# Kernel tuning notes

Hardware: AMD Instinct MI355X
Metric: run time of the kernel (lower is better)

## Reference

```python
import jax, jax.numpy as jnp
import numpy as np

N = 20000
IN_C = 512
HID = 64
H1 = 8
OUT_C = 256
E = 320000
NEG_SLOPE = 0.2


def gat_conv(x, src, dst, W, a_src, a_dst, b, concat):
    # PyG GATConv (shared lin for src/dst), inference mode (no dropout).
    H, C = a_src.shape
    h = (x @ W).reshape(N, H, C)                      # [N,H,C]
    alpha_src = (h * a_src[None]).sum(-1)             # [N,H]
    alpha_dst = (h * a_dst[None]).sum(-1)             # [N,H]
    alpha = jax.nn.leaky_relu(alpha_src[src] + alpha_dst[dst], NEG_SLOPE)  # [E,H]
    # segment softmax over incoming edges of each dst node
    amax = jax.ops.segment_max(alpha, dst, num_segments=N)
    amax = jnp.where(jnp.isfinite(amax), amax, 0.0)
    ex = jnp.exp(alpha - amax[dst])
    denom = jax.ops.segment_sum(ex, dst, num_segments=N)
    coef = ex / (denom[dst] + 1e-16)                  # [E,H]
    msg = h[src] * coef[:, :, None]                   # [E,H,C]
    out = jax.ops.segment_sum(msg, dst, num_segments=N)  # [N,H,C]
    out = out.reshape(N, H * C) if concat else out.mean(axis=1)
    return out + b


def setup_inputs() -> dict:
    key = jax.random.key(0)
    ks = jax.random.split(key, 10)
    x = jax.random.normal(ks[0], (N, IN_C), dtype=jnp.float32)
    edge_index = jax.random.randint(ks[1], (2, E), 0, N, dtype=jnp.int32)
    s1 = 1.0 / np.sqrt(IN_C)
    s2 = 1.0 / np.sqrt(HID * H1)
    W1 = jax.random.uniform(ks[2], (IN_C, H1 * HID), jnp.float32, -s1, s1)
    att_src1 = jax.random.uniform(ks[3], (H1, HID), jnp.float32, -s1, s1)
    att_dst1 = jax.random.uniform(ks[4], (H1, HID), jnp.float32, -s1, s1)
    b1 = jnp.zeros((H1 * HID,), jnp.float32)
    W2 = jax.random.uniform(ks[5], (H1 * HID, OUT_C), jnp.float32, -s2, s2)
    att_src2 = jax.random.uniform(ks[6], (1, OUT_C), jnp.float32, -s2, s2)
    att_dst2 = jax.random.uniform(ks[7], (1, OUT_C), jnp.float32, -s2, s2)
    b2 = jnp.zeros((OUT_C,), jnp.float32)
    return {"x": x, "edge_index": edge_index, "W1": W1, "att_src1": att_src1,
            "att_dst1": att_dst1, "b1": b1, "W2": W2, "att_src2": att_src2,
            "att_dst2": att_dst2, "b2": b2}


def reference(x, edge_index, W1, att_src1, att_dst1, b1, W2, att_src2, att_dst2, b2):
    # add self-loops (PyG GATConv default add_self_loops=True)
    loop = jnp.arange(N, dtype=edge_index.dtype)
    src = jnp.concatenate([edge_index[0], loop])
    dst = jnp.concatenate([edge_index[1], loop])
    h = gat_conv(x, src, dst, W1, att_src1, att_dst1, b1, concat=True)
    h = jax.nn.elu(h)
    out = gat_conv(h, src, dst, W2, att_src2, att_dst2, b2, concat=False)
    return jax.nn.log_softmax(out, axis=1)
```

## Files before the change

### kernel.cpp

```cpp
#include <hip/hip_runtime.h>
#include <math.h>

#define N_NODES 20000
#define IN_CH   512
#define HID_TOT 512
#define OUT_CH  256
#define N_EDGE  320000
#define TOT_EDGE (N_EDGE + N_NODES)
#define EPAD    400000

typedef __attribute__((ext_vector_type(8))) short short8;
typedef __attribute__((ext_vector_type(4))) float f32x4;
typedef __attribute__((ext_vector_type(2))) float f32x2;

__device__ __forceinline__ ushort f2bf(float f) {
    union { float f; unsigned u; } v; v.f = f;
    unsigned u = v.u;
    return (ushort)((u + 0x7fffu + ((u >> 16) & 1u)) >> 16);
}

__device__ __forceinline__ void glds16(const ushort* g, ushort* l) {
    __builtin_amdgcn_global_load_lds(
        (const __attribute__((address_space(1))) void*)g,
        (__attribute__((address_space(3))) void*)l, 16, 0, 0);
}

__device__ __forceinline__ float lrelu(float a) { return fmaxf(a, 0.2f * a); }

#define NA_BLK (N_NODES * IN_CH / 4 / 256)
#define NB_BLK ((IN_CH / 64) * (HID_TOT / 4))
#define NC_BLK ((HID_TOT / 64) * (OUT_CH / 4))
#define NZ_BLK ((N_NODES + 255) / 256)
__global__ __launch_bounds__(256) void prep_kernel(const float* __restrict__ x,
                                                   ushort* __restrict__ xb,
                                                   const float* __restrict__ W1,
                                                   ushort* __restrict__ w1t,
                                                   const float* __restrict__ W2,
                                                   ushort* __restrict__ w2t,
                                                   int* __restrict__ counts,
                                                   float* __restrict__ as2,
                                                   float* __restrict__ ad2) {
    int b = blockIdx.x;
    int t = threadIdx.x;
    if (b < NA_BLK) {
        int i = b * 256 + t;
        float4 v = *(const float4*)&x[(size_t)i * 4];
        ushort4 o = make_ushort4(f2bf(v.x), f2bf(v.y), f2bf(v.z), f2bf(v.w));
        *(ushort4*)&xb[(size_t)i * 4] = o;
    } else if (b < NA_BLK + NB_BLK) {
        int bb = b - NA_BLK;
        int k = (bb & 7) * 64 + (t & 63);
        int n = (bb >> 3) * 4 + (t >> 6);
        w1t[(size_t)n * IN_CH + k] = f2bf(W1[(size_t)k * HID_TOT + n]);
    } else if (b < NA_BLK + NB_BLK + NC_BLK) {
        int bb = b - NA_BLK - NB_BLK;
        int k = (bb & 7) * 64 + (t & 63);
        int n = (bb >> 3) * 4 + (t >> 6);
        w2t[(size_t)n * HID_TOT + k] = f2bf(W2[(size_t)k * OUT_CH + n]);
    } else {
        int i = (b - NA_BLK - NB_BLK - NC_BLK) * 256 + t;
        if (i < N_NODES) { counts[i] = 0; as2[i] = 0.f; ad2[i] = 0.f; }
    }
}

__global__ void hist_kernel(const int* __restrict__ ei, int* __restrict__ counts) {
    int e = blockIdx.x * blockDim.x + threadIdx.x;
    if (e >= TOT_EDGE) return;
    int d = (e < N_EDGE) ? ei[N_EDGE + e] : (e - N_EDGE);
    atomicAdd(&counts[d], 1);
}

__global__ __launch_bounds__(1024) void scan_kernel(const int* __restrict__ counts,
                                                    int* __restrict__ offsets,
                                                    int* __restrict__ cursors) {
    const int C = (N_NODES + 1023) / 1024;
    int t = threadIdx.x;
    int lane = t & 63, wid = t >> 6;
    int base = t * C;
    int sum = 0;
#pragma unroll
    for (int i = 0; i < C; i++) {
        int idx = base + i;
        if (idx < N_NODES) sum += (counts[idx] + 3) & ~3;
    }
    int val = sum;
#pragma unroll
    for (int off = 1; off < 64; off <<= 1) {
        int y = __shfl_up(val, off);
        if (lane >= off) val += y;
    }
    __shared__ int wsum[16], woff[16], stotal;
    if (lane == 63) wsum[wid] = val;
    __syncthreads();
    if (t == 0) {
        int r = 0;
        for (int w = 0; w < 16; w++) { woff[w] = r; r += wsum[w]; }
        stotal = r;
    }
    __syncthreads();
    int running = woff[wid] + (val - sum);
#pragma unroll
    for (int i = 0; i < C; i++) {
        int idx = base + i;
        if (idx < N_NODES) {
            offsets[idx] = running;
            cursors[idx] = running;
            running += (counts[idx] + 3) & ~3;
        }
    }
    if (t == 0) offsets[N_NODES] = stotal;
}

__global__ void scatter_kernel(const int* __restrict__ ei, int* __restrict__ cursors,
                               int* __restrict__ srcs, int* __restrict__ dsts) {
    int e = blockIdx.x * blockDim.x + threadIdx.x;
    if (e >= TOT_EDGE) return;
    int s, d;
    if (e < N_EDGE) { s = ei[e]; d = ei[N_EDGE + e]; } else { s = e - N_EDGE; d = s; }
    int pos = atomicAdd(&cursors[d], 1);
    srcs[pos] = s;
    dsts[pos] = d;
}

__global__ void pad_kernel(const int* __restrict__ cursors, const int* __restrict__ offsets,
                           int* __restrict__ srcs, int* __restrict__ dsts) {
    int v = blockIdx.x * blockDim.x + threadIdx.x;
    if (v >= N_NODES) return;
    int a = cursors[v], b = offsets[v + 1];
    for (int p = a; p < b; p++) { srcs[p] = 0; dsts[p] = -1; }
}

__global__ __launch_bounds__(256, 2) void gemm_mfma_kernel(const ushort* __restrict__ A,
                                                           const ushort* __restrict__ Bt,
                                                           unsigned char* __restrict__ Cf8,
                                                           const float* __restrict__ asrc,
                                                           const float* __restrict__ adst,
                                                           float* __restrict__ as_out,
                                                           float* __restrict__ ad_out,
                                                           int M, int N, int K, int layer1) {
    __shared__ ushort As[128 * 64];
    __shared__ ushort Bs[128 * 64];
    int t = threadIdx.x;
    int lane = t & 63;
    int wave = t >> 6;
    int wr = (wave >> 1) * 64;
    int wc = (wave & 1) * 64;
    int bm = blockIdx.y * 128, bn = blockIdx.x * 128;
    int q = lane >> 4, l15 = lane & 15;

    const ushort* Aptr[4]; ushort* Alds[4];
    const ushort* Bptr[4]; ushort* Blds[4];
#pragma unroll
    for (int k = 0; k < 4; k++) {
        int c = t + 256 * k;
        int r = c >> 3, kqs = c & 7;
        int kqg = kqs ^ (r & 7);
        int ar = bm + r; if (ar >= M) ar = M - 1;
        Aptr[k] = A + (size_t)ar * K + kqg * 8;
        Alds[k] = &As[c * 8];
        Bptr[k] = Bt + (size_t)(bn + r) * K + kqg * 8;
        Blds[k] = &Bs[c * 8];
    }

    f32x4 acc[4][4];
#pragma unroll
    for (int i = 0; i < 4; i++)
#pragma unroll
        for (int j = 0; j < 4; j++) acc[i][j] = f32x4{0.f, 0.f, 0.f, 0.f};

    for (int k0 = 0; k0 < K; k0 += 64) {
        __syncthreads();
        glds16(Aptr[0] + k0, Alds[0]);
        glds16(Aptr[1] + k0, Alds[1]);
        glds16(Aptr[2] + k0, Alds[2]);
        glds16(Aptr[3] + k0, Alds[3]);
        glds16(Bptr[0] + k0, Blds[0]);
        glds16(Bptr[1] + k0, Blds[1]);
        glds16(Bptr[2] + k0, Blds[2]);
        glds16(Bptr[3] + k0, Blds[3]);
        __syncthreads();

#pragma unroll
        for (int s = 0; s < 2; s++) {
            int kq = s * 4 + q;
            short8 af[4], bf[4];
#pragma unroll
            for (int i = 0; i < 4; i++) {
                int row = wr + i * 16 + l15;
                int slot = kq ^ (row & 7);
                af[i] = *(const short8*)&As[row * 64 + slot * 8];
            }
#pragma unroll
            for (int j = 0; j < 4; j++) {
                int row = wc + j * 16 + l15;
                int slot = kq ^ (row & 7);
                bf[j] = *(const short8*)&Bs[row * 64 + slot * 8];
            }
#pragma unroll
            for (int i = 0; i < 4; i++)
#pragma unroll
                for (int j = 0; j < 4; j++)
                    acc[i][j] = __builtin_amdgcn_mfma_f32_16x16x32_bf16(af[i], bf[j], acc[i][j], 0, 0, 0);
        }
    }

    float av[4], dv[4];
#pragma unroll
    for (int j = 0; j < 4; j++) {
        int cg = bn + wc + j * 16 + l15;
        av[j] = asrc[cg];
        dv[j] = adst[cg];
    }
    float ps[4][4], pd[4][4];
#pragma unroll
    for (int i = 0; i < 4; i++)
#pragma unroll
        for (int r = 0; r < 4; r++) {
            float p = 0.f, d = 0.f;
#pragma unroll
            for (int j = 0; j < 4; j++) {
                p = fmaf(acc[i][j][r], av[j], p);
                d = fmaf(acc[i][j][r], dv[j], d);
            }
            ps[i][r] = p; pd[i][r] = d;
        }
#pragma unroll
    for (int off = 1; off < 16; off <<= 1) {
#pragma unroll
        for (int i = 0; i < 4; i++)
#pragma unroll
            for (int r = 0; r < 4; r++) {
                ps[i][r] += __shfl_xor(ps[i][r], off);
                pd[i][r] += __shfl_xor(pd[i][r], off);
            }
    }

    int hidx = blockIdx.x * 2 + (wave & 1);
#pragma unroll
    for (int i = 0; i < 4; i++) {
#pragma unroll
        for (int r = 0; r < 4; r++) {
            int rg = bm + wr + i * 16 + q * 4 + r;
            if (rg < M) {
#pragma unroll
                for (int j = 0; j < 4; j++) {
                    int cg = bn + wc + j * 16 + l15;
                    int w8 = __builtin_amdgcn_cvt_pk_fp8_f32(acc[i][j][r], acc[i][j][r], 0, false);
                    Cf8[(size_t)rg * N + cg] = (unsigned char)(w8 & 0xff);
                }
                if (l15 == 0) {
                    if (layer1) {
                        as_out[rg * 8 + hidx] = ps[i][r];
                        ad_out[rg * 8 + hidx] = pd[i][r];
                    } else {
                        atomicAdd(&as_out[rg], ps[i][r]);
                        atomicAdd(&ad_out[rg], pd[i][r]);
                    }
                }
            }
        }
    }
}

__global__ __launch_bounds__(256) void wk1_kernel(const int* __restrict__ srcs,
                                                  const int* __restrict__ dsts,
                                                  const float* __restrict__ as1,
                                                  const float* __restrict__ ad1,
                                                  const int* __restrict__ offsets,
                                                  float* __restrict__ w1) {
    int pos = blockIdx.x * 256 + threadIdx.x;
    int tot = offsets[N_NODES];
    if (pos >= tot) return;
    int d = dsts[pos];
    if (d < 0) {
#pragma unroll
        for (int h = 0; h < 8; h++) w1[h * EPAD + pos] = 0.f;
        return;
    }
    int s = srcs[pos];
    float4 a0 = *(const float4*)&as1[(size_t)s * 8];
    float4 a1 = *(const float4*)&as1[(size_t)s * 8 + 4];
    float4 d0 = *(const float4*)&ad1[(size_t)d * 8];
    float4 d1 = *(const float4*)&ad1[(size_t)d * 8 + 4];
    w1[0 * EPAD + pos] = __expf(lrelu(a0.x + d0.x));
    w1[1 * EPAD + pos] = __expf(lrelu(a0.y + d0.y));
    w1[2 * EPAD + pos] = __expf(lrelu(a0.z + d0.z));
    w1[3 * EPAD + pos] = __expf(lrelu(a0.w + d0.w));
    w1[4 * EPAD + pos] = __expf(lrelu(a1.x + d1.x));
    w1[5 * EPAD + pos] = __expf(lrelu(a1.y + d1.y));
    w1[6 * EPAD + pos] = __expf(lrelu(a1.z + d1.z));
    w1[7 * EPAD + pos] = __expf(lrelu(a1.w + d1.w));
}

__global__ __launch_bounds__(256) void wk2_kernel(const int* __restrict__ srcs,
                                                  const int* __restrict__ dsts,
                                                  const float* __restrict__ as2,
                                                  const float* __restrict__ ad2,
                                                  const int* __restrict__ offsets,
                                                  float* __restrict__ w2) {
    int pos = blockIdx.x * 256 + threadIdx.x;
    int tot = offsets[N_NODES];
    if (pos >= tot) return;
    int d = dsts[pos];
    if (d < 0) { w2[pos] = 0.f; return; }
    w2[pos] = __expf(lrelu(as2[srcs[pos]] + ad2[d]));
}

__global__ __launch_bounds__(64) void agg1_kernel(const unsigned char* __restrict__ h1f,
                                                  const float* __restrict__ w1,
                                                  const int* __restrict__ offsets,
                                                  const int* __restrict__ srcs,
                                                  const float* __restrict__ b1,
                                                  ushort* __restrict__ h1ab) {
    int b = blockIdx.x;
    int head = b & 7;
    int grp = b >> 3;
    int lane = threadIdx.x;
    int sub = lane >> 3;
    int l8 = lane & 7;
    int v = grp * 8 + sub;
    int cofs = head * 64 + l8 * 8;
    const unsigned char* hb = h1f + cofs;
    const float* wh = w1 + head * EPAD;
    int s = offsets[v], e = offsets[v + 1];

    float denom = 0.f;
    float acc[8];
#pragma unroll
    for (int k = 0; k < 8; k++) acc[k] = 0.f;

    int i = s;
    for (; i + 8 <= e; i += 8) {
        int4 s0 = *(const int4*)&srcs[i];
        int4 s1 = *(const int4*)&srcs[i + 4];
        float4 w0 = *(const float4*)&wh[i];
        float4 w1v = *(const float4*)&wh[i + 4];
        uint2 r[8];
        r[0] = *(const uint2*)&hb[(size_t)s0.x * HID_TOT];
        r[1] = *(const uint2*)&hb[(size_t)s0.y * HID_TOT];
        r[2] = *(const uint2*)&hb[(size_t)s0.z * HID_TOT];
        r[3] = *(const uint2*)&hb[(size_t)s0.w * HID_TOT];
        r[4] = *(const uint2*)&hb[(size_t)s1.x * HID_TOT];
        r[5] = *(const uint2*)&hb[(size_t)s1.y * HID_TOT];
        r[6] = *(const uint2*)&hb[(size_t)s1.z * HID_TOT];
        r[7] = *(const uint2*)&hb[(size_t)s1.w * HID_TOT];
        float ww[8] = {w0.x, w0.y, w0.z, w0.w, w1v.x, w1v.y, w1v.z, w1v.w};
        denom += (w0.x + w0.y) + (w0.z + w0.w) + (w1v.x + w1v.y) + (w1v.z + w1v.w);
#pragma unroll
        for (int j = 0; j < 8; j++) {
            f32x2 pa = __builtin_amdgcn_cvt_pk_f32_fp8(r[j].x, false);
            f32x2 pb = __builtin_amdgcn_cvt_pk_f32_fp8(r[j].x, true);
            f32x2 pc = __builtin_amdgcn_cvt_pk_f32_fp8(r[j].y, false);
            f32x2 pdd = __builtin_amdgcn_cvt_pk_f32_fp8(r[j].y, true);
            acc[0] = fmaf(ww[j], pa.x, acc[0]); acc[1] = fmaf(ww[j], pa.y, acc[1]);
            acc[2] = fmaf(ww[j], pb.x, acc[2]); acc[3] = fmaf(ww[j], pb.y, acc[3]);
            acc[4] = fmaf(ww[j], pc.x, acc[4]); acc[5] = fmaf(ww[j], pc.y, acc[5]);
            acc[6] = fmaf(ww[j], pdd.x, acc[6]); acc[7] = fmaf(ww[j], pdd.y, acc[7]);
        }
    }
    if (i < e) {
        int4 s0 = *(const int4*)&srcs[i];
        float4 w0 = *(const float4*)&wh[i];
        uint2 r[4];
        r[0] = *(const uint2*)&hb[(size_t)s0.x * HID_TOT];
        r[1] = *(const uint2*)&hb[(size_t)s0.y * HID_TOT];
        r[2] = *(const uint2*)&hb[(size_t)s0.z * HID_TOT];
        r[3] = *(const uint2*)&hb[(size_t)s0.w * HID_TOT];
        float ww[4] = {w0.x, w0.y, w0.z, w0.w};
        denom += (w0.x + w0.y) + (w0.z + w0.w);
#pragma unroll
        for (int j = 0; j < 4; j++) {
            f32x2 pa = __builtin_amdgcn_cvt_pk_f32_fp8(r[j].x, false);
            f32x2 pb = __builtin_amdgcn_cvt_pk_f32_fp8(r[j].x, true);
            f32x2 pc = __builtin_amdgcn_cvt_pk_f32_fp8(r[j].y, false);
            f32x2 pdd = __builtin_amdgcn_cvt_pk_f32_fp8(r[j].y, true);
            acc[0] = fmaf(ww[j], pa.x, acc[0]); acc[1] = fmaf(ww[j], pa.y, acc[1]);
            acc[2] = fmaf(ww[j], pb.x, acc[2]); acc[3] = fmaf(ww[j], pb.y, acc[3]);
            acc[4] = fmaf(ww[j], pc.x, acc[4]); acc[5] = fmaf(ww[j], pc.y, acc[5]);
            acc[6] = fmaf(ww[j], pdd.x, acc[6]); acc[7] = fmaf(ww[j], pdd.y, acc[7]);
        }
    }

    float inv = 1.f / (denom + 1e-16f);
    short8 ov;
#pragma unroll
    for (int k = 0; k < 8; k++) {
        float o = acc[k] * inv + b1[cofs + k];
        o = (o > 0.f) ? o : expm1f(o);
        ov[k] = (short)f2bf(o);
    }
    *(short8*)&h1ab[(size_t)v * HID_TOT + cofs] = ov;
}

__global__ __launch_bounds__(64) void agg2_kernel(const unsigned char* __restrict__ h2f,
                                                  const float* __restrict__ w2,
                                                  const int* __restrict__ offsets,
                                                  const int* __restrict__ srcs,
                                                  const float* __restrict__ b2,
                                                  float* __restrict__ out) {
    int lane = threadIdx.x;
    int sub = lane >> 5;
    int l32 = lane & 31;
    int v = blockIdx.x * 2 + sub;
    int c8 = l32 * 8;
    const unsigned char* hb = h2f + c8;
    int s = offsets[v], e = offsets[v + 1];

    float denom = 0.f;
    float acc[8];
#pragma unroll
    for (int k = 0; k < 8; k++) acc[k] = 0.f;

    int i = s;
    for (; i + 8 <= e; i += 8) {
        int4 s0 = *(const int4*)&srcs[i];
        int4 s1 = *(const int4*)&srcs[i + 4];
        float4 w0 = *(const float4*)&w2[i];
        float4 w1v = *(const float4*)&w2[i + 4];
        uint2 r[8];
        r[0] = *(const uint2*)&hb[(size_t)s0.x * OUT_CH];
        r[1] = *(const uint2*)&hb[(size_t)s0.y * OUT_CH];
        r[2] = *(const uint2*)&hb[(size_t)s0.z * OUT_CH];
        r[3] = *(const uint2*)&hb[(size_t)s0.w * OUT_CH];
        r[4] = *(const uint2*)&hb[(size_t)s1.x * OUT_CH];
        r[5] = *(const uint2*)&hb[(size_t)s1.y * OUT_CH];
        r[6] = *(const uint2*)&hb[(size_t)s1.z * OUT_CH];
        r[7] = *(const uint2*)&hb[(size_t)s1.w * OUT_CH];
        float ww[8] = {w0.x, w0.y, w0.z, w0.w, w1v.x, w1v.y, w1v.z, w1v.w};
        denom += (w0.x + w0.y) + (w0.z + w0.w) + (w1v.x + w1v.y) + (w1v.z + w1v.w);
#pragma unroll
        for (int j = 0; j < 8; j++) {
            f32x2 pa = __builtin_amdgcn_cvt_pk_f32_fp8(r[j].x, false);
            f32x2 pb = __builtin_amdgcn_cvt_pk_f32_fp8(r[j].x, true);
            f32x2 pc = __builtin_amdgcn_cvt_pk_f32_fp8(r[j].y, false);
            f32x2 pdd = __builtin_amdgcn_cvt_pk_f32_fp8(r[j].y, true);
            acc[0] = fmaf(ww[j], pa.x, acc[0]); acc[1] = fmaf(ww[j], pa.y, acc[1]);
            acc[2] = fmaf(ww[j], pb.x, acc[2]); acc[3] = fmaf(ww[j], pb.y, acc[3]);
            acc[4] = fmaf(ww[j], pc.x, acc[4]); acc[5] = fmaf(ww[j], pc.y, acc[5]);
            acc[6] = fmaf(ww[j], pdd.x, acc[6]); acc[7] = fmaf(ww[j], pdd.y, acc[7]);
        }
    }
    if (i < e) {
        int4 s0 = *(const int4*)&srcs[i];
        float4 w0 = *(const float4*)&w2[i];
        uint2 r[4];
        r[0] = *(const uint2*)&hb[(size_t)s0.x * OUT_CH];
        r[1] = *(const uint2*)&hb[(size_t)s0.y * OUT_CH];
        r[2] = *(const uint2*)&hb[(size_t)s0.z * OUT_CH];
        r[3] = *(const uint2*)&hb[(size_t)s0.w * OUT_CH];
        float ww[4] = {w0.x, w0.y, w0.z, w0.w};
        denom += (w0.x + w0.y) + (w0.z + w0.w);
#pragma unroll
        for (int j = 0; j < 4; j++) {
            f32x2 pa = __builtin_amdgcn_cvt_pk_f32_fp8(r[j].x, false);
            f32x2 pb = __builtin_amdgcn_cvt_pk_f32_fp8(r[j].x, true);
            f32x2 pc = __builtin_amdgcn_cvt_pk_f32_fp8(r[j].y, false);
            f32x2 pdd = __builtin_amdgcn_cvt_pk_f32_fp8(r[j].y, true);
            acc[0] = fmaf(ww[j], pa.x, acc[0]); acc[1] = fmaf(ww[j], pa.y, acc[1]);
            acc[2] = fmaf(ww[j], pb.x, acc[2]); acc[3] = fmaf(ww[j], pb.y, acc[3]);
            acc[4] = fmaf(ww[j], pc.x, acc[4]); acc[5] = fmaf(ww[j], pc.y, acc[5]);
            acc[6] = fmaf(ww[j], pdd.x, acc[6]); acc[7] = fmaf(ww[j], pdd.y, acc[7]);
        }
    }

    float inv = 1.f / (denom + 1e-16f);
    float xv[8];
#pragma unroll
    for (int k = 0; k < 8; k++) xv[k] = acc[k] * inv + b2[c8 + k];

    float mm = xv[0];
#pragma unroll
    for (int k = 1; k < 8; k++) mm = fmaxf(mm, xv[k]);
#pragma unroll
    for (int off = 1; off < 32; off <<= 1) mm = fmaxf(mm, __shfl_xor(mm, off));
    float sum = 0.f;
#pragma unroll
    for (int k = 0; k < 8; k++) sum += __expf(xv[k] - mm);
#pragma unroll
    for (int off = 1; off < 32; off <<= 1) sum += __shfl_xor(sum, off);
    float ls = logf(sum);
    float4 o0, o1;
    o0.x = xv[0] - mm - ls; o0.y = xv[1] - mm - ls;
    o0.z = xv[2] - mm - ls; o0.w = xv[3] - mm - ls;
    o1.x = xv[4] - mm - ls; o1.y = xv[5] - mm - ls;
    o1.z = xv[6] - mm - ls; o1.w = xv[7] - mm - ls;
    *(float4*)&out[(size_t)v * OUT_CH + c8] = o0;
    *(float4*)&out[(size_t)v * OUT_CH + c8 + 4] = o1;
}

static inline size_t align256(size_t x) { return (x + 255) & ~(size_t)255; }

extern "C" void kernel_launch(void* const* d_in, const int* in_sizes, int n_in,
                              void* d_out, int out_size, void* d_ws, size_t ws_size,
                              hipStream_t stream) {
    const float* x    = (const float*)d_in[0];
    const int*   ei   = (const int*)d_in[1];
    const float* W1   = (const float*)d_in[2];
    const float* as1w = (const float*)d_in[3];
    const float* ad1w = (const float*)d_in[4];
    const float* b1   = (const float*)d_in[5];
    const float* W2   = (const float*)d_in[6];
    const float* as2w = (const float*)d_in[7];
    const float* ad2w = (const float*)d_in[8];
    const float* b2   = (const float*)d_in[9];
    float* out = (float*)d_out;

    char* p = (char*)d_ws;
    unsigned char* h1f = (unsigned char*)p; p += align256((size_t)N_NODES * HID_TOT);
    unsigned char* h2f = (unsigned char*)p; p += align256((size_t)N_NODES * OUT_CH);
    ushort* xb   = (ushort*)p; p += align256(sizeof(ushort) * (size_t)N_NODES * IN_CH);
    ushort* h1ab = xb;
    ushort* w1t  = (ushort*)p; p += align256(sizeof(ushort) * (size_t)IN_CH * HID_TOT);
    ushort* w2t  = (ushort*)p; p += align256(sizeof(ushort) * (size_t)HID_TOT * OUT_CH);
    float* as1  = (float*)p; p += align256(sizeof(float) * (size_t)N_NODES * 8);
    float* ad1  = (float*)p; p += align256(sizeof(float) * (size_t)N_NODES * 8);
    float* as2  = (float*)p; p += align256(sizeof(float) * (size_t)N_NODES);
    float* ad2  = (float*)p; p += align256(sizeof(float) * (size_t)N_NODES);
    int* counts  = (int*)p; p += align256(sizeof(int) * (size_t)N_NODES);
    int* offsets = (int*)p; p += align256(sizeof(int) * (size_t)(N_NODES + 1));
    int* cursors = (int*)p; p += align256(sizeof(int) * (size_t)N_NODES);
    int* srcs    = (int*)p; p += align256(sizeof(int) * (size_t)EPAD);
    int* dsts    = (int*)p; p += align256(sizeof(int) * (size_t)EPAD);
    float* w1    = (float*)p; p += align256(sizeof(float) * (size_t)EPAD * 8);
    float* w2    = (float*)p; p += align256(sizeof(float) * (size_t)EPAD);

    prep_kernel<<<NA_BLK + NB_BLK + NC_BLK + NZ_BLK, 256, 0, stream>>>(
        x, xb, W1, w1t, W2, w2t, counts, as2, ad2);

    int eb = (TOT_EDGE + 255) / 256;
    hist_kernel<<<eb, 256, 0, stream>>>(ei, counts);
    scan_kernel<<<1, 1024, 0, stream>>>(counts, offsets, cursors);
    scatter_kernel<<<eb, 256, 0, stream>>>(ei, cursors, srcs, dsts);
    pad_kernel<<<(N_NODES + 255) / 256, 256, 0, stream>>>(cursors, offsets, srcs, dsts);

    int wb = (EPAD + 255) / 256;
    gemm_mfma_kernel<<<dim3(HID_TOT / 128, (N_NODES + 127) / 128), 256, 0, stream>>>(
        xb, w1t, h1f, as1w, ad1w, as1, ad1, N_NODES, HID_TOT, IN_CH, 1);
    wk1_kernel<<<wb, 256, 0, stream>>>(srcs, dsts, as1, ad1, offsets, w1);
    agg1_kernel<<<2500 * 8, 64, 0, stream>>>(h1f, w1, offsets, srcs, b1, h1ab);

    gemm_mfma_kernel<<<dim3(OUT_CH / 128, (N_NODES + 127) / 128), 256, 0, stream>>>(
        h1ab, w2t, h2f, as2w, ad2w, as2, ad2, N_NODES, OUT_CH, HID_TOT, 0);
    wk2_kernel<<<wb, 256, 0, stream>>>(srcs, dsts, as2, ad2, offsets, w2);
    agg2_kernel<<<N_NODES / 2, 64, 0, stream>>>(h2f, w2, offsets, srcs, b2, out);
}
```

Before: 284.9 us.

## Fuse edge-weight computation into aggregation kernels and degree-sort node order

Removes the separate wk1/wk2 kernels that wrote per-edge exp weights to global memory; each aggregation lane now computes one edge's weight from head-major attention scores and broadcasts it by shuffle. Padding slots point to a sentinel node with a -1e30 score and zero features, which removes the dsts array and the pad kernel. The scan kernel also builds a degree-bucketed permutation so each block processes nodes of similar degree, reducing divergence. It also adds software prefetch of the next source indices. This cuts global traffic and launches at the cost of extra exp and shuffle work inside the aggregation loops.

```diff
diff --git a/kernel.cpp b/kernel.cpp
--- a/kernel.cpp
+++ b/kernel.cpp
@@ -2,6 +2,7 @@
 #include <math.h>
 
 #define N_NODES 20000
+#define NP1     20001
 #define IN_CH   512
 #define HID_TOT 512
 #define OUT_CH  256
@@ -38,8 +39,11 @@
                                                    const float* __restrict__ W2,
                                                    ushort* __restrict__ w2t,
                                                    int* __restrict__ counts,
+                                                   float* __restrict__ as1,
                                                    float* __restrict__ as2,
-                                                   float* __restrict__ ad2) {
+                                                   float* __restrict__ ad2,
+                                                   unsigned char* __restrict__ h1f,
+                                                   unsigned char* __restrict__ h2f) {
     int b = blockIdx.x;
     int t = threadIdx.x;
     if (b < NA_BLK) {
@@ -60,6 +64,10 @@
     } else {
         int i = (b - NA_BLK - NB_BLK - NC_BLK) * 256 + t;
         if (i < N_NODES) { counts[i] = 0; as2[i] = 0.f; ad2[i] = 0.f; }
+        if (i == N_NODES) as2[N_NODES] = -1e30f;
+        if (i < 8) as1[(size_t)i * NP1 + N_NODES] = -1e30f;
+        if (i < 128) ((unsigned*)(h1f + (size_t)N_NODES * HID_TOT))[i] = 0u;
+        if (i < 64)  ((unsigned*)(h2f + (size_t)N_NODES * OUT_CH))[i] = 0u;
     }
 }
 
@@ -72,7 +80,9 @@
 
 __global__ __launch_bounds__(1024) void scan_kernel(const int* __restrict__ counts,
                                                     int* __restrict__ offsets,
-                                                    int* __restrict__ cursors) {
+                                                    int* __restrict__ cursors,
+                                                    int* __restrict__ srcs,
+                                                    int* __restrict__ perm) {
     const int C = (N_NODES + 1023) / 1024;
     int t = threadIdx.x;
     int lane = t & 63, wid = t >> 6;
@@ -90,7 +100,9 @@
         if (lane >= off) val += y;
     }
     __shared__ int wsum[16], woff[16], stotal;
+    __shared__ int bins[64];
     if (lane == 63) wsum[wid] = val;
+    if (t < 64) bins[t] = 0;
     __syncthreads();
     if (t == 0) {
         int r = 0;
@@ -105,29 +117,48 @@
         if (idx < N_NODES) {
             offsets[idx] = running;
             cursors[idx] = running;
-            running += (counts[idx] + 3) & ~3;
+            int real = counts[idx];
+            int padded = (real + 3) & ~3;
+            for (int pp = running + real; pp < running + padded; pp++)
+                srcs[pp] = N_NODES;
+            running += padded;
         }
     }
     if (t == 0) offsets[N_NODES] = stotal;
+
+#pragma unroll
+    for (int i = 0; i < C; i++) {
+        int idx = base + i;
+        if (idx < N_NODES) {
+            int d = counts[idx]; if (d > 63) d = 63;
+            atomicAdd(&bins[d], 1);
+        }
+    }
+    __syncthreads();
+    if (t == 0) {
+        int r = 0;
+        for (int d = 0; d < 64; d++) { int c = bins[d]; bins[d] = r; r += c; }
+    }
+    __syncthreads();
+#pragma unroll
+    for (int i = 0; i < C; i++) {
+        int idx = base + i;
+        if (idx < N_NODES) {
+            int d = counts[idx]; if (d > 63) d = 63;
+            int pos = atomicAdd(&bins[d], 1);
+            perm[pos] = idx;
+        }
+    }
 }
 
 __global__ void scatter_kernel(const int* __restrict__ ei, int* __restrict__ cursors,
-                               int* __restrict__ srcs, int* __restrict__ dsts) {
+                               int* __restrict__ srcs) {
     int e = blockIdx.x * blockDim.x + threadIdx.x;
     if (e >= TOT_EDGE) return;
     int s, d;
     if (e < N_EDGE) { s = ei[e]; d = ei[N_EDGE + e]; } else { s = e - N_EDGE; d = s; }
     int pos = atomicAdd(&cursors[d], 1);
     srcs[pos] = s;
-    dsts[pos] = d;
-}
-
-__global__ void pad_kernel(const int* __restrict__ cursors, const int* __restrict__ offsets,
-                           int* __restrict__ srcs, int* __restrict__ dsts) {
-    int v = blockIdx.x * blockDim.x + threadIdx.x;
-    if (v >= N_NODES) return;
-    int a = cursors[v], b = offsets[v + 1];
-    for (int p = a; p < b; p++) { srcs[p] = 0; dsts[p] = -1; }
 }
 
 __global__ __launch_bounds__(256, 2) void gemm_mfma_kernel(const ushort* __restrict__ A,
@@ -250,8 +281,8 @@
                 }
                 if (l15 == 0) {
                     if (layer1) {
-                        as_out[rg * 8 + hidx] = ps[i][r];
-                        ad_out[rg * 8 + hidx] = pd[i][r];
+                        as_out[(size_t)hidx * NP1 + rg] = ps[i][r];
+                        ad_out[(size_t)hidx * NP1 + rg] = pd[i][r];
                     } else {
                         atomicAdd(&as_out[rg], ps[i][r]);
                         atomicAdd(&ad_out[rg], pd[i][r]);
@@ -262,54 +293,12 @@
     }
 }
 
-__global__ __launch_bounds__(256) void wk1_kernel(const int* __restrict__ srcs,
-                                                  const int* __restrict__ dsts,
+__global__ __launch_bounds__(64) void agg1_kernel(const unsigned char* __restrict__ h1f,
                                                   const float* __restrict__ as1,
                                                   const float* __restrict__ ad1,
                                                   const int* __restrict__ offsets,
-                                                  float* __restrict__ w1) {
-    int pos = blockIdx.x * 256 + threadIdx.x;
-    int tot = offsets[N_NODES];
-    if (pos >= tot) return;
-    int d = dsts[pos];
-    if (d < 0) {
-#pragma unroll
-        for (int h = 0; h < 8; h++) w1[h * EPAD + pos] = 0.f;
-        return;
-    }
-    int s = srcs[pos];
-    float4 a0 = *(const float4*)&as1[(size_t)s * 8];
-    float4 a1 = *(const float4*)&as1[(size_t)s * 8 + 4];
-    float4 d0 = *(const float4*)&ad1[(size_t)d * 8];
-    float4 d1 = *(const float4*)&ad1[(size_t)d * 8 + 4];
-    w1[0 * EPAD + pos] = __expf(lrelu(a0.x + d0.x));
-    w1[1 * EPAD + pos] = __expf(lrelu(a0.y + d0.y));
-    w1[2 * EPAD + pos] = __expf(lrelu(a0.z + d0.z));
-    w1[3 * EPAD + pos] = __expf(lrelu(a0.w + d0.w));
-    w1[4 * EPAD + pos] = __expf(lrelu(a1.x + d1.x));
-    w1[5 * EPAD + pos] = __expf(lrelu(a1.y + d1.y));
-    w1[6 * EPAD + pos] = __expf(lrelu(a1.z + d1.z));
-    w1[7 * EPAD + pos] = __expf(lrelu(a1.w + d1.w));
-}
-
-__global__ __launch_bounds__(256) void wk2_kernel(const int* __restrict__ srcs,
-                                                  const int* __restrict__ dsts,
-                                                  const float* __restrict__ as2,
-                                                  const float* __restrict__ ad2,
-                                                  const int* __restrict__ offsets,
-                                                  float* __restrict__ w2) {
-    int pos = blockIdx.x * 256 + threadIdx.x;
-    int tot = offsets[N_NODES];
-    if (pos >= tot) return;
-    int d = dsts[pos];
-    if (d < 0) { w2[pos] = 0.f; return; }
-    w2[pos] = __expf(lrelu(as2[srcs[pos]] + ad2[d]));
-}
-
-__global__ __launch_bounds__(64) void agg1_kernel(const unsigned char* __restrict__ h1f,
-                                                  const float* __restrict__ w1,
-                                                  const int* __restrict__ offsets,
                                                   const int* __restrict__ srcs,
+                                                  const int* __restrict__ perm,
                                                   const float* __restrict__ b1,
                                                   ushort* __restrict__ h1ab) {
     int b = blockIdx.x;
@@ -318,10 +307,11 @@
     int lane = threadIdx.x;
     int sub = lane >> 3;
     int l8 = lane & 7;
-    int v = grp * 8 + sub;
+    int v = perm[grp * 8 + sub];
     int cofs = head * 64 + l8 * 8;
     const unsigned char* hb = h1f + cofs;
-    const float* wh = w1 + head * EPAD;
+    const float* as1h = as1 + (size_t)head * NP1;
+    float adv = ad1[(size_t)head * NP1 + v];
     int s = offsets[v], e = offsets[v + 1];
 
     float denom = 0.f;
@@ -330,22 +320,36 @@
     for (int k = 0; k < 8; k++) acc[k] = 0.f;
 
     int i = s;
-    for (; i + 8 <= e; i += 8) {
-        int4 s0 = *(const int4*)&srcs[i];
-        int4 s1 = *(const int4*)&srcs[i + 4];
-        float4 w0 = *(const float4*)&wh[i];
-        float4 w1v = *(const float4*)&wh[i + 4];
+    int4 cs0 = {0, 0, 0, 0}, cs1 = {0, 0, 0, 0};
+    int csn = N_NODES;
+    if (i + 8 <= e) {
+        cs0 = *(const int4*)&srcs[i];
+        cs1 = *(const int4*)&srcs[i + 4];
+        csn = srcs[i + l8];
+    }
+    while (i + 8 <= e) {
         uint2 r[8];
-        r[0] = *(const uint2*)&hb[(size_t)s0.x * HID_TOT];
-        r[1] = *(const uint2*)&hb[(size_t)s0.y * HID_TOT];
-        r[2] = *(const uint2*)&hb[(size_t)s0.z * HID_TOT];
-        r[3] = *(const uint2*)&hb[(size_t)s0.w * HID_TOT];
-        r[4] = *(const uint2*)&hb[(size_t)s1.x * HID_TOT];
-        r[5] = *(const uint2*)&hb[(size_t)s1.y * HID_TOT];
-        r[6] = *(const uint2*)&hb[(size_t)s1.z * HID_TOT];
-        r[7] = *(const uint2*)&hb[(size_t)s1.w * HID_TOT];
-        float ww[8] = {w0.x, w0.y, w0.z, w0.w, w1v.x, w1v.y, w1v.z, w1v.w};
-        denom += (w0.x + w0.y) + (w0.z + w0.w) + (w1v.x + w1v.y) + (w1v.z + w1v.w);
+        r[0] = *(const uint2*)&hb[(size_t)cs0.x * HID_TOT];
+        r[1] = *(const uint2*)&hb[(size_t)cs0.y * HID_TOT];
+        r[2] = *(const uint2*)&hb[(size_t)cs0.z * HID_TOT];
+        r[3] = *(const uint2*)&hb[(size_t)cs0.w * HID_TOT];
+        r[4] = *(const uint2*)&hb[(size_t)cs1.x * HID_TOT];
+        r[5] = *(const uint2*)&hb[(size_t)cs1.y * HID_TOT];
+        r[6] = *(const uint2*)&hb[(size_t)cs1.z * HID_TOT];
+        r[7] = *(const uint2*)&hb[(size_t)cs1.w * HID_TOT];
+        float aown = as1h[csn];
+        int ni = i + 8;
+        int4 ns0 = cs0, ns1 = cs1; int nsn = csn;
+        if (ni + 8 <= e) {
+            ns0 = *(const int4*)&srcs[ni];
+            ns1 = *(const int4*)&srcs[ni + 4];
+            nsn = srcs[ni + l8];
+        }
+        float w_own = __expf(lrelu(aown + adv));
+        denom += w_own;
+        float ww[8];
+#pragma unroll
+        for (int j = 0; j < 8; j++) ww[j] = __shfl(w_own, (lane & 56) | j);
 #pragma unroll
         for (int j = 0; j < 8; j++) {
             f32x2 pa = __builtin_amdgcn_cvt_pk_f32_fp8(r[j].x, false);
@@ -357,17 +361,21 @@
             acc[4] = fmaf(ww[j], pc.x, acc[4]); acc[5] = fmaf(ww[j], pc.y, acc[5]);
             acc[6] = fmaf(ww[j], pdd.x, acc[6]); acc[7] = fmaf(ww[j], pdd.y, acc[7]);
         }
+        cs0 = ns0; cs1 = ns1; csn = nsn; i = ni;
     }
     if (i < e) {
         int4 s0 = *(const int4*)&srcs[i];
-        float4 w0 = *(const float4*)&wh[i];
+        int snt = srcs[i + (l8 & 3)];
         uint2 r[4];
         r[0] = *(const uint2*)&hb[(size_t)s0.x * HID_TOT];
         r[1] = *(const uint2*)&hb[(size_t)s0.y * HID_TOT];
         r[2] = *(const uint2*)&hb[(size_t)s0.z * HID_TOT];
         r[3] = *(const uint2*)&hb[(size_t)s0.w * HID_TOT];
-        float ww[4] = {w0.x, w0.y, w0.z, w0.w};
-        denom += (w0.x + w0.y) + (w0.z + w0.w);
+        float w_own = __expf(lrelu(as1h[snt] + adv));
+        if (l8 < 4) denom += w_own;
+        float ww[4];
+#pragma unroll
+        for (int j = 0; j < 4; j++) ww[j] = __shfl(w_own, (lane & 56) | j);
 #pragma unroll
         for (int j = 0; j < 4; j++) {
             f32x2 pa = __builtin_amdgcn_cvt_pk_f32_fp8(r[j].x, false);
@@ -381,6 +389,10 @@
         }
     }
 
+    denom += __shfl_xor(denom, 1);
+    denom += __shfl_xor(denom, 2);
+    denom += __shfl_xor(denom, 4);
+
     float inv = 1.f / (denom + 1e-16f);
     short8 ov;
 #pragma unroll
@@ -393,17 +405,20 @@
 }
 
 __global__ __launch_bounds__(64) void agg2_kernel(const unsigned char* __restrict__ h2f,
-                                                  const float* __restrict__ w2,
+                                                  const float* __restrict__ as2,
+                                                  const float* __restrict__ ad2,
                                                   const int* __restrict__ offsets,
                                                   const int* __restrict__ srcs,
+                                                  const int* __restrict__ perm,
                                                   const float* __restrict__ b2,
                                                   float* __restrict__ out) {
     int lane = threadIdx.x;
     int sub = lane >> 5;
     int l32 = lane & 31;
-    int v = blockIdx.x * 2 + sub;
+    int v = perm[blockIdx.x * 2 + sub];
     int c8 = l32 * 8;
     const unsigned char* hb = h2f + c8;
+    float adv = ad2[v];
     int s = offsets[v], e = offsets[v + 1];
 
     float denom = 0.f;
@@ -412,22 +427,36 @@
     for (int k = 0; k < 8; k++) acc[k] = 0.f;
 
     int i = s;
-    for (; i + 8 <= e; i += 8) {
-        int4 s0 = *(const int4*)&srcs[i];
-        int4 s1 = *(const int4*)&srcs[i + 4];
-        float4 w0 = *(const float4*)&w2[i];
-        float4 w1v = *(const float4*)&w2[i + 4];
+    int4 cs0 = {0, 0, 0, 0}, cs1 = {0, 0, 0, 0};
+    int csn = N_NODES;
+    if (i + 8 <= e) {
+        cs0 = *(const int4*)&srcs[i];
+        cs1 = *(const int4*)&srcs[i + 4];
+        csn = srcs[i + (l32 & 7)];
+    }
+    while (i + 8 <= e) {
         uint2 r[8];
-        r[0] = *(const uint2*)&hb[(size_t)s0.x * OUT_CH];
-        r[1] = *(const uint2*)&hb[(size_t)s0.y * OUT_CH];
-        r[2] = *(const uint2*)&hb[(size_t)s0.z * OUT_CH];
-        r[3] = *(const uint2*)&hb[(size_t)s0.w * OUT_CH];
-        r[4] = *(const uint2*)&hb[(size_t)s1.x * OUT_CH];
-        r[5] = *(const uint2*)&hb[(size_t)s1.y * OUT_CH];
-        r[6] = *(const uint2*)&hb[(size_t)s1.z * OUT_CH];
-        r[7] = *(const uint2*)&hb[(size_t)s1.w * OUT_CH];
-        float ww[8] = {w0.x, w0.y, w0.z, w0.w, w1v.x, w1v.y, w1v.z, w1v.w};
-        denom += (w0.x + w0.y) + (w0.z + w0.w) + (w1v.x + w1v.y) + (w1v.z + w1v.w);
+        r[0] = *(const uint2*)&hb[(size_t)cs0.x * OUT_CH];
+        r[1] = *(const uint2*)&hb[(size_t)cs0.y * OUT_CH];
+        r[2] = *(const uint2*)&hb[(size_t)cs0.z * OUT_CH];
+        r[3] = *(const uint2*)&hb[(size_t)cs0.w * OUT_CH];
+        r[4] = *(const uint2*)&hb[(size_t)cs1.x * OUT_CH];
+        r[5] = *(const uint2*)&hb[(size_t)cs1.y * OUT_CH];
+        r[6] = *(const uint2*)&hb[(size_t)cs1.z * OUT_CH];
+        r[7] = *(const uint2*)&hb[(size_t)cs1.w * OUT_CH];
+        float aown = as2[csn];
+        int ni = i + 8;
+        int4 ns0 = cs0, ns1 = cs1; int nsn = csn;
+        if (ni + 8 <= e) {
+            ns0 = *(const int4*)&srcs[ni];
+            ns1 = *(const int4*)&srcs[ni + 4];
+            nsn = srcs[ni + (l32 & 7)];
+        }
+        float w_own = __expf(lrelu(aown + adv));
+        if (l32 < 8) denom += w_own;
+        float ww[8];
+#pragma unroll
+        for (int j = 0; j < 8; j++) ww[j] = __shfl(w_own, (lane & 32) | j);
 #pragma unroll
         for (int j = 0; j < 8; j++) {
             f32x2 pa = __builtin_amdgcn_cvt_pk_f32_fp8(r[j].x, false);
@@ -439,17 +468,21 @@
             acc[4] = fmaf(ww[j], pc.x, acc[4]); acc[5] = fmaf(ww[j], pc.y, acc[5]);
             acc[6] = fmaf(ww[j], pdd.x, acc[6]); acc[7] = fmaf(ww[j], pdd.y, acc[7]);
         }
+        cs0 = ns0; cs1 = ns1; csn = nsn; i = ni;
     }
     if (i < e) {
         int4 s0 = *(const int4*)&srcs[i];
-        float4 w0 = *(const float4*)&w2[i];
+        int snt = srcs[i + (l32 & 3)];
         uint2 r[4];
         r[0] = *(const uint2*)&hb[(size_t)s0.x * OUT_CH];
         r[1] = *(const uint2*)&hb[(size_t)s0.y * OUT_CH];
         r[2] = *(const uint2*)&hb[(size_t)s0.z * OUT_CH];
         r[3] = *(const uint2*)&hb[(size_t)s0.w * OUT_CH];
-        float ww[4] = {w0.x, w0.y, w0.z, w0.w};
-        denom += (w0.x + w0.y) + (w0.z + w0.w);
+        float w_own = __expf(lrelu(as2[snt] + adv));
+        if (l32 < 4) denom += w_own;
+        float ww[4];
+#pragma unroll
+        for (int j = 0; j < 4; j++) ww[j] = __shfl(w_own, (lane & 32) | j);
 #pragma unroll
         for (int j = 0; j < 4; j++) {
             f32x2 pa = __builtin_amdgcn_cvt_pk_f32_fp8(r[j].x, false);
@@ -462,6 +495,12 @@
             acc[6] = fmaf(ww[j], pdd.x, acc[6]); acc[7] = fmaf(ww[j], pdd.y, acc[7]);
         }
     }
+
+    denom += __shfl_xor(denom, 1);
+    denom += __shfl_xor(denom, 2);
+    denom += __shfl_xor(denom, 4);
+    denom += __shfl_xor(denom, 8);
+    denom += __shfl_xor(denom, 16);
 
     float inv = 1.f / (denom + 1e-16f);
     float xv[8];
@@ -506,41 +545,35 @@
     float* out = (float*)d_out;
 
     char* p = (char*)d_ws;
-    unsigned char* h1f = (unsigned char*)p; p += align256((size_t)N_NODES * HID_TOT);
-    unsigned char* h2f = (unsigned char*)p; p += align256((size_t)N_NODES * OUT_CH);
+    unsigned char* h1f = (unsigned char*)p; p += align256((size_t)NP1 * HID_TOT);
+    unsigned char* h2f = (unsigned char*)p; p += align256((size_t)NP1 * OUT_CH);
     ushort* xb   = (ushort*)p; p += align256(sizeof(ushort) * (size_t)N_NODES * IN_CH);
     ushort* h1ab = xb;
     ushort* w1t  = (ushort*)p; p += align256(sizeof(ushort) * (size_t)IN_CH * HID_TOT);
     ushort* w2t  = (ushort*)p; p += align256(sizeof(ushort) * (size_t)HID_TOT * OUT_CH);
-    float* as1  = (float*)p; p += align256(sizeof(float) * (size_t)N_NODES * 8);
-    float* ad1  = (float*)p; p += align256(sizeof(float) * (size_t)N_NODES * 8);
-    float* as2  = (float*)p; p += align256(sizeof(float) * (size_t)N_NODES);
-    float* ad2  = (float*)p; p += align256(sizeof(float) * (size_t)N_NODES);
+    float* as1  = (float*)p; p += align256(sizeof(float) * (size_t)NP1 * 8);
+    float* ad1  = (float*)p; p += align256(sizeof(float) * (size_t)NP1 * 8);
+    float* as2  = (float*)p; p += align256(sizeof(float) * (size_t)NP1);
+    float* ad2  = (float*)p; p += align256(sizeof(float) * (size_t)NP1);
     int* counts  = (int*)p; p += align256(sizeof(int) * (size_t)N_NODES);
     int* offsets = (int*)p; p += align256(sizeof(int) * (size_t)(N_NODES + 1));
     int* cursors = (int*)p; p += align256(sizeof(int) * (size_t)N_NODES);
+    int* perm    = (int*)p; p += align256(sizeof(int) * (size_t)N_NODES);
     int* srcs    = (int*)p; p += align256(sizeof(int) * (size_t)EPAD);
-    int* dsts    = (int*)p; p += align256(sizeof(int) * (size_t)EPAD);
-    float* w1    = (float*)p; p += align256(sizeof(float) * (size_t)EPAD * 8);
-    float* w2    = (float*)p; p += align256(sizeof(float) * (size_t)EPAD);
 
     prep_kernel<<<NA_BLK + NB_BLK + NC_BLK + NZ_BLK, 256, 0, stream>>>(
-        x, xb, W1, w1t, W2, w2t, counts, as2, ad2);
+        x, xb, W1, w1t, W2, w2t, counts, as1, as2, ad2, h1f, h2f);
 
     int eb = (TOT_EDGE + 255) / 256;
     hist_kernel<<<eb, 256, 0, stream>>>(ei, counts);
-    scan_kernel<<<1, 1024, 0, stream>>>(counts, offsets, cursors);
-    scatter_kernel<<<eb, 256, 0, stream>>>(ei, cursors, srcs, dsts);
-    pad_kernel<<<(N_NODES + 255) / 256, 256, 0, stream>>>(cursors, offsets, srcs, dsts);
-
-    int wb = (EPAD + 255) / 256;
+    scan_kernel<<<1, 1024, 0, stream>>>(counts, offsets, cursors, srcs, perm);
+    scatter_kernel<<<eb, 256, 0, stream>>>(ei, cursors, srcs);
+
     gemm_mfma_kernel<<<dim3(HID_TOT / 128, (N_NODES + 127) / 128), 256, 0, stream>>>(
         xb, w1t, h1f, as1w, ad1w, as1, ad1, N_NODES, HID_TOT, IN_CH, 1);
-    wk1_kernel<<<wb, 256, 0, stream>>>(srcs, dsts, as1, ad1, offsets, w1);
-    agg1_kernel<<<2500 * 8, 64, 0, stream>>>(h1f, w1, offsets, srcs, b1, h1ab);
+    agg1_kernel<<<2500 * 8, 64, 0, stream>>>(h1f, as1, ad1, offsets, srcs, perm, b1, h1ab);
 
     gemm_mfma_kernel<<<dim3(OUT_CH / 128, (N_NODES + 127) / 128), 256, 0, stream>>>(
         h1ab, w2t, h2f, as2w, ad2w, as2, ad2, N_NODES, OUT_CH, HID_TOT, 0);
-    wk2_kernel<<<wb, 256, 0, stream>>>(srcs, dsts, as2, ad2, offsets, w2);
-    agg2_kernel<<<N_NODES / 2, 64, 0, stream>>>(h2f, w2, offsets, srcs, b2, out);
-}
+    agg2_kernel<<<N_NODES / 2, 64, 0, stream>>>(h2f, as2, ad2, offsets, srcs, perm, b2, out);
+}
```

Measured after the change: 305.2 us. 7.1% more time.
